# Performance work log

Measured on AMD Instinct MI355X. Metric: run time of the kernel, lower is better.

## Reference

```python
import jax, jax.numpy as jnp
import numpy as np

N = 50000      # nodes
E = 800000     # edges (before self-loops)
IN = 128       # in_channels
C = 64         # hidden_channels
HD = 4         # heads
SLOPE = 0.2    # GATConv leaky_relu negative slope
EPS_BN = 1e-5


def add_self_loops(edge_index, n):
    loop = jnp.arange(n, dtype=edge_index.dtype)
    return jnp.concatenate([edge_index, jnp.stack([loop, loop])], axis=1)


def gat_conv(x, edge_index, W, a_src, a_dst, bias, heads, out_c, concat, n):
    src, dst = edge_index[0], edge_index[1]
    h = (x @ W).reshape(n, heads, out_c)                 # [N,H,C]
    al_s = jnp.sum(h * a_src, axis=-1)                   # [N,H]
    al_d = jnp.sum(h * a_dst, axis=-1)                   # [N,H]
    e = jax.nn.leaky_relu(al_s[src] + al_d[dst], SLOPE)  # [Etot,H]
    m = jax.ops.segment_max(e, dst, num_segments=n)      # segment softmax (stable)
    ex = jnp.exp(e - m[dst])
    s = jax.ops.segment_sum(ex, dst, num_segments=n)
    alpha = ex / (s[dst] + 1e-16)                        # [Etot,H]
    out = jax.ops.segment_sum(h[src] * alpha[:, :, None], dst, num_segments=n)
    out = out.reshape(n, heads * out_c) if concat else out.mean(axis=1)
    return out + bias


def batch_norm(x, gamma, beta):
    mu = x.mean(axis=0)
    var = x.var(axis=0)
    return (x - mu) * jax.lax.rsqrt(var + EPS_BN) * gamma + beta


def setup_inputs() -> dict:
    key = jax.random.key(0)
    ks = jax.random.split(key, 24)
    f = lambda k, shp, sc: (jax.random.normal(k, shp, dtype=jnp.float32) * sc)
    HC = HD * C
    return {
        "x": f(ks[0], (N, IN), 1.0),
        "edge_index": jax.random.randint(ks[1], (2, E), 0, N, dtype=jnp.int64),
        # conv1: IN -> C, heads=HD, concat
        "W1": f(ks[2], (IN, HC), 0.05), "as1": f(ks[3], (HD, C), 0.05),
        "ad1": f(ks[4], (HD, C), 0.05), "b1": f(ks[5], (HC,), 0.02),
        "g1": jnp.ones((HC,), jnp.float32), "bb1": jnp.zeros((HC,), jnp.float32),
        # conv2: HC -> C, heads=HD, concat
        "W2": f(ks[6], (HC, HC), 0.05), "as2": f(ks[7], (HD, C), 0.05),
        "ad2": f(ks[8], (HD, C), 0.05), "b2": f(ks[9], (HC,), 0.02),
        "g2": jnp.ones((HC,), jnp.float32), "bb2": jnp.zeros((HC,), jnp.float32),
        # conv3: HC -> C, heads=1, mean
        "W3": f(ks[10], (HC, C), 0.05), "as3": f(ks[11], (1, C), 0.05),
        "ad3": f(ks[12], (1, C), 0.05), "b3": f(ks[13], (C,), 0.02),
        # skips
        "Ws1": f(ks[14], (IN, HC), 0.05), "bs1": f(ks[15], (HC,), 0.02),
        "Ws2": f(ks[16], (HC, C), 0.05), "bs2": f(ks[17], (C,), 0.02),
    }


def reference(x, edge_index, W1, as1, ad1, b1, g1, bb1,
              W2, as2, ad2, b2, g2, bb2,
              W3, as3, ad3, b3, Ws1, bs1, Ws2, bs2):
    ei = add_self_loops(edge_index, N)
    x_init = x @ Ws1 + bs1
    h = gat_conv(x, ei, W1, as1, ad1, b1, HD, C, True, N)
    h = jax.nn.elu(batch_norm(h, g1, bb1)) + x_init
    x_skip = h @ Ws2 + bs2
    h = gat_conv(h, ei, W2, as2, ad2, b2, HD, C, True, N)
    h = jax.nn.elu(batch_norm(h, g2, bb2))
    out = gat_conv(h, ei, W3, as3, ad3, b3, 1, C, False, N) + x_skip
    return out
```

## Files before the change

### kernel.cpp

```cpp
#include <hip/hip_runtime.h>
#include <hip/hip_bf16.h>
#include <cstdint>
#include <cstddef>


#define LRELU_SLOPE 0.2f

typedef __attribute__((ext_vector_type(8))) short short8;
typedef __attribute__((ext_vector_type(4))) float f32x4;

__device__ __forceinline__ float bf2f(unsigned short u) {
  union { unsigned int i; float f; } t; t.i = ((unsigned int)u) << 16; return t.f;
}
__device__ __forceinline__ unsigned short f2bf(float f) {
  __hip_bfloat16 h = __float2bfloat16(f);
  return *reinterpret_cast<unsigned short*>(&h);
}

template<int K, int WAVES_GAT, int WAVES_SKIP>
__global__ __launch_bounds__((WAVES_GAT + WAVES_SKIP) * 64)
void gemm_gat_fused(const unsigned short* __restrict__ A,
                    const unsigned short* __restrict__ BtH,
                    const unsigned short* __restrict__ BtS,
                    const float* __restrict__ a_s, const float* __restrict__ a_d,
                    const float* __restrict__ biasS,
                    unsigned short* __restrict__ Hout,
                    float* __restrict__ als, float* __restrict__ ald,
                    unsigned short* __restrict__ Sout, int M) {
  constexpr int NKS = K / 32;
  constexpr int NH  = WAVES_GAT * 64;
  constexpr int NS  = WAVES_SKIP * 64;
  const int wid  = threadIdx.x >> 6;
  const int lane = threadIdx.x & 63;
  const int r    = lane & 15;
  const int q    = lane >> 4;
  const int koff = q * 8;
  const bool isGat = wid < WAVES_GAT;
  const int colbase = isGat ? wid * 64 : (wid - WAVES_GAT) * 64;
  const unsigned short* Bt = isGat ? BtH : BtS;

  short8 b[4][NKS];
  #pragma unroll
  for (int nf = 0; nf < 4; ++nf)
    #pragma unroll
    for (int ks = 0; ks < NKS; ++ks)
      b[nf][ks] = *(const short8*)(Bt + (size_t)(colbase + nf * 16 + r) * K + ks * 32 + koff);

  float as4[4] = {}, ad4[4] = {};
  if (isGat) {
    #pragma unroll
    for (int nf = 0; nf < 4; ++nf) {
      as4[nf] = a_s[colbase + nf * 16 + r];
      ad4[nf] = a_d[colbase + nf * 16 + r];
    }
  }

  const int ntiles = (M + 15) >> 4;
  const int chunk = (ntiles + 7) >> 3;
  const int xcd   = blockIdx.x & 7;
  const int lo    = xcd * chunk;
  const int hi    = min(lo + chunk, ntiles);
  const int bstep = gridDim.x >> 3;
  for (int t = lo + (blockIdx.x >> 3); t < hi; t += bstep) {
    const int row = t * 16 + r;
    short8 a[NKS];
    #pragma unroll
    for (int ks = 0; ks < NKS; ++ks) {
      a[ks] = (short8)(short)0;
      if (row < M) a[ks] = *(const short8*)(A + (size_t)row * K + ks * 32 + koff);
    }
    f32x4 acc[4];
    #pragma unroll
    for (int nf = 0; nf < 4; ++nf) acc[nf] = (f32x4)0.0f;
    #pragma unroll
    for (int ks = 0; ks < NKS; ++ks)
      #pragma unroll
      for (int nf = 0; nf < 4; ++nf)
        acc[nf] = __builtin_amdgcn_mfma_f32_16x16x32_bf16(a[ks], b[nf][ks], acc[nf], 0, 0, 0);

    const int rbase = t * 16 + q * 4;
    if (isGat) {
      #pragma unroll
      for (int nf = 0; nf < 4; ++nf) {
        const int col = colbase + nf * 16 + r;
        #pragma unroll
        for (int i = 0; i < 4; ++i) {
          const int rr = rbase + i;
          if (rr < M) Hout[(size_t)rr * NH + col] = f2bf(acc[nf][i]);
        }
      }
      #pragma unroll
      for (int i = 0; i < 4; ++i) {
        float s = 0.f, d = 0.f;
        #pragma unroll
        for (int nf = 0; nf < 4; ++nf) {
          s = fmaf(acc[nf][i], as4[nf], s);
          d = fmaf(acc[nf][i], ad4[nf], d);
        }
        #pragma unroll
        for (int m = 8; m >= 1; m >>= 1) {
          s += __shfl_xor(s, m, 64);
          d += __shfl_xor(d, m, 64);
        }
        const int rr = rbase + i;
        if (r == 0 && rr < M) {
          als[(size_t)rr * WAVES_GAT + wid] = s;
          ald[(size_t)rr * WAVES_GAT + wid] = d;
        }
      }
    } else {
      #pragma unroll
      for (int nf = 0; nf < 4; ++nf) {
        const int col = colbase + nf * 16 + r;
        const float bs = biasS[col];
        #pragma unroll
        for (int i = 0; i < 4; ++i) {
          const int rr = rbase + i;
          if (rr < M) Sout[(size_t)rr * NS + col] = f2bf(acc[nf][i] + bs);
        }
      }
    }
  }
}

__global__ __launch_bounds__(256)
void gemm_gat3(const unsigned short* __restrict__ A, const unsigned short* __restrict__ Bt,
               const float* __restrict__ a_s, const float* __restrict__ a_d,
               unsigned short* __restrict__ Hout, float* __restrict__ als,
               float* __restrict__ ald, int M) {
  constexpr int K = 256, NKS = 8;
  const int wid  = threadIdx.x >> 6;
  const int lane = threadIdx.x & 63;
  const int r    = lane & 15;
  const int q    = lane >> 4;
  const int koff = q * 8;

  short8 b[4][NKS];
  #pragma unroll
  for (int nf = 0; nf < 4; ++nf)
    #pragma unroll
    for (int ks = 0; ks < NKS; ++ks)
      b[nf][ks] = *(const short8*)(Bt + (size_t)(nf * 16 + r) * K + ks * 32 + koff);
  float as4[4], ad4[4];
  #pragma unroll
  for (int nf = 0; nf < 4; ++nf) {
    as4[nf] = a_s[nf * 16 + r];
    ad4[nf] = a_d[nf * 16 + r];
  }

  const int ntiles = (M + 15) >> 4;
  const int chunk = (ntiles + 7) >> 3;
  const int xcd   = blockIdx.x & 7;
  const int lo    = xcd * chunk;
  const int hi    = min(lo + chunk, ntiles);
  const int bstep = (gridDim.x >> 3) * 4;
  for (int t = lo + (blockIdx.x >> 3) * 4 + wid; t < hi; t += bstep) {
    const int row = t * 16 + r;
    short8 a[NKS];
    #pragma unroll
    for (int ks = 0; ks < NKS; ++ks) {
      a[ks] = (short8)(short)0;
      if (row < M) a[ks] = *(const short8*)(A + (size_t)row * K + ks * 32 + koff);
    }
    f32x4 acc[4];
    #pragma unroll
    for (int nf = 0; nf < 4; ++nf) acc[nf] = (f32x4)0.0f;
    #pragma unroll
    for (int ks = 0; ks < NKS; ++ks)
      #pragma unroll
      for (int nf = 0; nf < 4; ++nf)
        acc[nf] = __builtin_amdgcn_mfma_f32_16x16x32_bf16(a[ks], b[nf][ks], acc[nf], 0, 0, 0);

    const int rbase = t * 16 + q * 4;
    #pragma unroll
    for (int nf = 0; nf < 4; ++nf) {
      const int col = nf * 16 + r;
      #pragma unroll
      for (int i = 0; i < 4; ++i) {
        const int rr = rbase + i;
        if (rr < M) Hout[(size_t)rr * 64 + col] = f2bf(acc[nf][i]);
      }
    }
    #pragma unroll
    for (int i = 0; i < 4; ++i) {
      float s = 0.f, d = 0.f;
      #pragma unroll
      for (int nf = 0; nf < 4; ++nf) {
        s = fmaf(acc[nf][i], as4[nf], s);
        d = fmaf(acc[nf][i], ad4[nf], d);
      }
      #pragma unroll
      for (int m = 8; m >= 1; m >>= 1) {
        s += __shfl_xor(s, m, 64);
        d += __shfl_xor(d, m, 64);
      }
      const int rr = rbase + i;
      if (r == 0 && rr < M) { als[rr] = s; ald[rr] = d; }
    }
  }
}

__global__ __launch_bounds__(256)
void prep_all(const float* __restrict__ x,
              const float* __restrict__ W1, const float* __restrict__ Ws1,
              const float* __restrict__ W2, const float* __restrict__ Ws2,
              const float* __restrict__ W3,
              unsigned short* __restrict__ xb,
              unsigned short* __restrict__ W1t, unsigned short* __restrict__ Ws1t,
              unsigned short* __restrict__ W2t, unsigned short* __restrict__ Ws2t,
              unsigned short* __restrict__ W3t, int n) {
  int idx = blockIdx.x * blockDim.x + threadIdx.x;
  const int nx = n * 32;
  if (idx < nx) {
    float4 v = ((const float4*)x)[idx];
    ushort4 o;
    o.x = f2bf(v.x); o.y = f2bf(v.y); o.z = f2bf(v.z); o.w = f2bf(v.w);
    ((ushort4*)xb)[idx] = o;
    return;
  }
  idx -= nx;
  if (idx < 256 * 128) { int nn = idx >> 7, kk = idx & 127; W1t[idx]  = f2bf(W1[kk * 256 + nn]);  return; }
  idx -= 256 * 128;
  if (idx < 256 * 128) { int nn = idx >> 7, kk = idx & 127; Ws1t[idx] = f2bf(Ws1[kk * 256 + nn]); return; }
  idx -= 256 * 128;
  if (idx < 256 * 256) { int nn = idx >> 8, kk = idx & 255; W2t[idx]  = f2bf(W2[kk * 256 + nn]);  return; }
  idx -= 256 * 256;
  if (idx < 64 * 256)  { int nn = idx >> 8, kk = idx & 255; Ws2t[idx] = f2bf(Ws2[kk * 64 + nn]);  return; }
  idx -= 64 * 256;
  if (idx < 64 * 256)  { int nn = idx >> 8, kk = idx & 255; W3t[idx]  = f2bf(W3[kk * 64 + nn]); }
}

__global__ void count_edges(const int* __restrict__ ei, int E, int* __restrict__ counts) {
  int i = blockIdx.x * blockDim.x + threadIdx.x;
  if (i < E) atomicAdd(&counts[ei[E + i]], 1);
}
__global__ void scan_block(const int* __restrict__ in, int* __restrict__ out,
                           int* __restrict__ bsums, int n) {
  __shared__ int tmp[256];
  int t = threadIdx.x;
  int gid = blockIdx.x * 256 + t;
  int v = (gid < n) ? in[gid] : 0;
  tmp[t] = v;
  __syncthreads();
  #pragma unroll
  for (int off = 1; off < 256; off <<= 1) {
    int x = (t >= off) ? tmp[t - off] : 0;
    __syncthreads();
    tmp[t] += x;
    __syncthreads();
  }
  if (gid < n) out[gid] = tmp[t] - v;
  if (t == 255) bsums[blockIdx.x] = tmp[255];
}
__global__ void scan_tops(const int* __restrict__ bsums, int* __restrict__ boffs, int nb) {
  __shared__ int tmp[256];
  int t = threadIdx.x;
  int v = (t < nb) ? bsums[t] : 0;
  tmp[t] = v;
  __syncthreads();
  #pragma unroll
  for (int off = 1; off < 256; off <<= 1) {
    int x = (t >= off) ? tmp[t - off] : 0;
    __syncthreads();
    tmp[t] += x;
    __syncthreads();
  }
  if (t < nb) boffs[t] = tmp[t] - v;
}
__global__ void scan_add(int* __restrict__ rp, const int* __restrict__ boffs,
                         int n, int etot) {
  int gid = blockIdx.x * 256 + threadIdx.x;
  if (gid < n) rp[gid] += boffs[blockIdx.x];
  if (gid == 0) rp[n] = etot;
}
__global__ void fill_edges(const int* __restrict__ ei, int E, const int* __restrict__ rp,
                           int* __restrict__ cursor, int* __restrict__ csr) {
  int i = blockIdx.x * blockDim.x + threadIdx.x;
  if (i < E) {
    int d = ei[E + i];
    int s = ei[i];
    int pos = rp[d] + atomicAdd(&cursor[d], 1);
    csr[pos] = s;
  }
}

template<int HEADS, int HCt, bool OUT_BF16>
__global__ __launch_bounds__(256)
void gat_aggregate(const unsigned short* __restrict__ H, const float* __restrict__ als,
                   const float* __restrict__ ald, const int* __restrict__ rp,
                   const int* __restrict__ csr, const float* __restrict__ bias,
                   const unsigned short* __restrict__ skip, void* __restrict__ out, int n) {
  constexpr int CPL = HCt / 64;
  int w = (blockIdx.x * blockDim.x + threadIdx.x) >> 6;
  int lane = threadIdx.x & 63;
  if (w >= n) return;
  const int beg = rp[w], end = rp[w + 1];
  const int myhead = (HEADS == 1) ? 0 : (lane >> 4);
  const float adh = ald[(size_t)w * HEADS + myhead];

  auto att = [&](int s) -> float {
    float e = als[(size_t)s * HEADS + myhead] + adh;
    e = fmaxf(e, LRELU_SLOPE * e);
    return __expf(e);
  };

  float acc[CPL];
  float ssum = att(w);
  {
    const unsigned short* hp = H + (size_t)w * HCt + lane * CPL;
    if constexpr (CPL == 4) {
      ushort4 hv = *(const ushort4*)hp;
      acc[0] = ssum * bf2f(hv.x); acc[1] = ssum * bf2f(hv.y);
      acc[2] = ssum * bf2f(hv.z); acc[3] = ssum * bf2f(hv.w);
    } else {
      acc[0] = ssum * bf2f(hp[0]);
    }
  }

  int j = beg;
  for (; j + 8 <= end; j += 8) {
    int sidx[8];
    #pragma unroll
    for (int u = 0; u < 8; ++u) sidx[u] = csr[j + u];
    if constexpr (CPL == 4) {
      ushort4 hv[8];
      #pragma unroll
      for (int u = 0; u < 8; ++u)
        hv[u] = *(const ushort4*)(H + (size_t)sidx[u] * HCt + lane * 4);
      float ex[8];
      #pragma unroll
      for (int u = 0; u < 8; ++u) ex[u] = att(sidx[u]);
      #pragma unroll
      for (int u = 0; u < 8; ++u) {
        ssum += ex[u];
        acc[0] = fmaf(ex[u], bf2f(hv[u].x), acc[0]);
        acc[1] = fmaf(ex[u], bf2f(hv[u].y), acc[1]);
        acc[2] = fmaf(ex[u], bf2f(hv[u].z), acc[2]);
        acc[3] = fmaf(ex[u], bf2f(hv[u].w), acc[3]);
      }
    } else {
      unsigned short hv[8];
      #pragma unroll
      for (int u = 0; u < 8; ++u) hv[u] = H[(size_t)sidx[u] * HCt + lane];
      float ex[8];
      #pragma unroll
      for (int u = 0; u < 8; ++u) ex[u] = att(sidx[u]);
      #pragma unroll
      for (int u = 0; u < 8; ++u) {
        ssum += ex[u];
        acc[0] = fmaf(ex[u], bf2f(hv[u]), acc[0]);
      }
    }
  }
  for (; j + 4 <= end; j += 4) {
    int sidx[4];
    #pragma unroll
    for (int u = 0; u < 4; ++u) sidx[u] = csr[j + u];
    float ex[4];
    #pragma unroll
    for (int u = 0; u < 4; ++u) ex[u] = att(sidx[u]);
    if constexpr (CPL == 4) {
      ushort4 hv[4];
      #pragma unroll
      for (int u = 0; u < 4; ++u)
        hv[u] = *(const ushort4*)(H + (size_t)sidx[u] * HCt + lane * 4);
      #pragma unroll
      for (int u = 0; u < 4; ++u) {
        ssum += ex[u];
        acc[0] = fmaf(ex[u], bf2f(hv[u].x), acc[0]);
        acc[1] = fmaf(ex[u], bf2f(hv[u].y), acc[1]);
        acc[2] = fmaf(ex[u], bf2f(hv[u].z), acc[2]);
        acc[3] = fmaf(ex[u], bf2f(hv[u].w), acc[3]);
      }
    } else {
      unsigned short hv[4];
      #pragma unroll
      for (int u = 0; u < 4; ++u) hv[u] = H[(size_t)sidx[u] * HCt + lane];
      #pragma unroll
      for (int u = 0; u < 4; ++u) {
        ssum += ex[u];
        acc[0] = fmaf(ex[u], bf2f(hv[u]), acc[0]);
      }
    }
  }
  for (; j < end; ++j) {
    const int s = csr[j];
    const float ex = att(s);
    ssum += ex;
    const unsigned short* hp = H + (size_t)s * HCt + lane * CPL;
    if constexpr (CPL == 4) {
      ushort4 hv = *(const ushort4*)hp;
      acc[0] = fmaf(ex, bf2f(hv.x), acc[0]);
      acc[1] = fmaf(ex, bf2f(hv.y), acc[1]);
      acc[2] = fmaf(ex, bf2f(hv.z), acc[2]);
      acc[3] = fmaf(ex, bf2f(hv.w), acc[3]);
    } else {
      acc[0] = fmaf(ex, bf2f(hp[0]), acc[0]);
    }
  }

  const float inv = 1.f / (ssum + 1e-16f);
  #pragma unroll
  for (int c = 0; c < CPL; ++c) {
    int ch = lane * CPL + c;
    float v = acc[c] * inv + bias[ch];
    if (skip) v += bf2f(skip[(size_t)w * HCt + ch]);
    if constexpr (OUT_BF16)
      ((unsigned short*)out)[(size_t)w * HCt + ch] = f2bf(v);
    else
      ((float*)out)[(size_t)w * HCt + ch] = v;
  }
}

__global__ __launch_bounds__(256)
void bn_stats(const unsigned short* __restrict__ X, float* __restrict__ sums, int n) {
  int c = threadIdx.x;
  float s = 0.f, q = 0.f;
  for (int r = blockIdx.x; r < n; r += gridDim.x) {
    float v = bf2f(X[(size_t)r * 256 + c]);
    s += v;
    q = fmaf(v, v, q);
  }
  atomicAdd(&sums[c], s);
  atomicAdd(&sums[256 + c], q);
}
__global__ void bn_finalize(const float* __restrict__ sums, const float* __restrict__ gamma,
                            const float* __restrict__ beta, float* __restrict__ scsh,
                            int n) {
  int c = threadIdx.x;
  if (c < 256) {
    float mean = sums[c] / (float)n;
    float var = sums[256 + c] / (float)n - mean * mean;
    float sc = gamma[c] * rsqrtf(var + 1e-5f);
    scsh[c] = sc;
    scsh[256 + c] = beta[c] - mean * sc;
  }
}
__global__ __launch_bounds__(256)
void bn_apply_elu(const unsigned short* __restrict__ X, const float* __restrict__ scsh,
                  const unsigned short* __restrict__ skip, unsigned short* __restrict__ Y,
                  int total) {
  int i4 = blockIdx.x * blockDim.x + threadIdx.x;
  if (i4 * 4 >= total) return;
  ushort4 xv = ((const ushort4*)X)[i4];
  int cb = (i4 * 4) & 255;
  float4 sc = *(const float4*)(scsh + cb);
  float4 sh = *(const float4*)(scsh + 256 + cb);
  float4 y;
  y.x = fmaf(bf2f(xv.x), sc.x, sh.x);
  y.y = fmaf(bf2f(xv.y), sc.y, sh.y);
  y.z = fmaf(bf2f(xv.z), sc.z, sh.z);
  y.w = fmaf(bf2f(xv.w), sc.w, sh.w);
  y.x = (y.x > 0.f) ? y.x : expm1f(y.x);
  y.y = (y.y > 0.f) ? y.y : expm1f(y.y);
  y.z = (y.z > 0.f) ? y.z : expm1f(y.z);
  y.w = (y.w > 0.f) ? y.w : expm1f(y.w);
  if (skip) {
    ushort4 s4 = ((const ushort4*)skip)[i4];
    y.x += bf2f(s4.x); y.y += bf2f(s4.y); y.z += bf2f(s4.z); y.w += bf2f(s4.w);
  }
  ushort4 o;
  o.x = f2bf(y.x); o.y = f2bf(y.y); o.z = f2bf(y.z); o.w = f2bf(y.w);
  ((ushort4*)Y)[i4] = o;
}

extern "C" void kernel_launch(void* const* d_in, const int* in_sizes, int n_in,
                              void* d_out, int out_size, void* d_ws, size_t ws_size,
                              hipStream_t stream) {
  const float* x   = (const float*)d_in[0];
  const int*   ei  = (const int*)d_in[1];
  const float* W1  = (const float*)d_in[2];
  const float* as1 = (const float*)d_in[3];
  const float* ad1 = (const float*)d_in[4];
  const float* b1  = (const float*)d_in[5];
  const float* g1  = (const float*)d_in[6];
  const float* bb1 = (const float*)d_in[7];
  const float* W2  = (const float*)d_in[8];
  const float* as2 = (const float*)d_in[9];
  const float* ad2 = (const float*)d_in[10];
  const float* b2  = (const float*)d_in[11];
  const float* g2  = (const float*)d_in[12];
  const float* bb2 = (const float*)d_in[13];
  const float* W3  = (const float*)d_in[14];
  const float* as3 = (const float*)d_in[15];
  const float* ad3 = (const float*)d_in[16];
  const float* b3  = (const float*)d_in[17];
  const float* Ws1 = (const float*)d_in[18];
  const float* bs1 = (const float*)d_in[19];
  const float* Ws2 = (const float*)d_in[20];
  const float* bs2 = (const float*)d_in[21];

  const int n = in_sizes[0] / 128;
  const int E = in_sizes[1] / 2;

  char* wsp = (char*)d_ws;
  auto carve = [&](size_t bytes) -> void* {
    void* p = (void*)wsp;
    wsp += (bytes + 255) & ~(size_t)255;
    return p;
  };
  unsigned short* Hb  = (unsigned short*)carve((size_t)n * 256 * 2);
  unsigned short* hb  = (unsigned short*)carve((size_t)n * 256 * 2);
  unsigned short* xbD = (unsigned short*)carve((size_t)n * 128 * 2);
  unsigned short* xb  = xbD;
  unsigned short* D   = xbD;
  unsigned short* Bv  = (unsigned short*)carve((size_t)n * 256 * 2);
  unsigned short* Cv  = (unsigned short*)carve((size_t)n * 256 * 2);
  float* als  = (float*)carve((size_t)n * 4 * 4);
  float* ald  = (float*)carve((size_t)n * 4 * 4);
  int*   rp   = (int*)carve((size_t)(n + 1) * 4);
  int*   cnt  = (int*)carve((size_t)n * 4);
  int*   bsums= (int*)carve(256 * 4);
  int*   boffs= (int*)carve(256 * 4);
  int*   csr  = (int*)carve((size_t)E * 4);
  float* bnb  = (float*)carve(4 * 256 * 4);
  float* sums = bnb;
  float* scsh = bnb + 512;
  unsigned short* W1t  = (unsigned short*)carve(128 * 256 * 2);
  unsigned short* Ws1t = (unsigned short*)carve(128 * 256 * 2);
  unsigned short* W2t  = (unsigned short*)carve(256 * 256 * 2);
  unsigned short* Ws2t = (unsigned short*)carve(256 * 64 * 2);
  unsigned short* W3t  = (unsigned short*)carve(256 * 64 * 2);

  const int NB = (n + 255) / 256;
  const int EB = (E + 255) / 256;

  hipMemsetAsync(cnt, 0, (size_t)n * 4, stream);
  count_edges<<<EB, 256, 0, stream>>>(ei, E, cnt);
  scan_block<<<NB, 256, 0, stream>>>(cnt, rp, bsums, n);
  scan_tops<<<1, 256, 0, stream>>>(bsums, boffs, NB);
  scan_add<<<NB, 256, 0, stream>>>(rp, boffs, n, E);
  hipMemsetAsync(cnt, 0, (size_t)n * 4, stream);
  fill_edges<<<EB, 256, 0, stream>>>(ei, E, rp, cnt, csr);

  {
    const int total = n * 32 + 2 * 256 * 128 + 256 * 256 + 2 * 64 * 256;
    prep_all<<<(total + 255) / 256, 256, 0, stream>>>(x, W1, Ws1, W2, Ws2, W3,
                                                      xb, W1t, Ws1t, W2t, Ws2t, W3t, n);
  }

  const int wgrid = (n * 64 + 255) / 256;
  const int egrid = (n * 256 / 4 + 255) / 256;

  gemm_gat_fused<128, 4, 4><<<512, 512, 0, stream>>>(
      xb, W1t, Ws1t, as1, ad1, bs1, Hb, als, ald, Bv, n);
  gat_aggregate<4, 256, true><<<wgrid, 256, 0, stream>>>(Hb, als, ald, rp, csr, b1,
                                                         nullptr, Cv, n);
  hipMemsetAsync(sums, 0, 512 * 4, stream);
  bn_stats<<<256, 256, 0, stream>>>(Cv, sums, n);
  bn_finalize<<<1, 256, 0, stream>>>(sums, g1, bb1, scsh, n);
  bn_apply_elu<<<egrid, 256, 0, stream>>>(Cv, scsh, Bv, hb, n * 256);

  gemm_gat_fused<256, 4, 1><<<512, 320, 0, stream>>>(
      hb, W2t, Ws2t, as2, ad2, bs2, Hb, als, ald, D, n);
  gat_aggregate<4, 256, true><<<wgrid, 256, 0, stream>>>(Hb, als, ald, rp, csr, b2,
                                                         nullptr, Cv, n);
  hipMemsetAsync(sums, 0, 512 * 4, stream);
  bn_stats<<<256, 256, 0, stream>>>(Cv, sums, n);
  bn_finalize<<<1, 256, 0, stream>>>(sums, g2, bb2, scsh, n);
  bn_apply_elu<<<egrid, 256, 0, stream>>>(Cv, scsh, nullptr, hb, n * 256);

  gemm_gat3<<<512, 256, 0, stream>>>(hb, W3t, as3, ad3, Hb, als, ald, n);
  gat_aggregate<1, 64, false><<<wgrid, 256, 0, stream>>>(Hb, als, ald, rp, csr, b3, D,
                                                         d_out, n);
}
```

Baseline: 515.2 us.

## Precompute per-edge attention exponentials in separate kernel before aggregation

```diff
diff --git a/kernel.cpp b/kernel.cpp
--- a/kernel.cpp
+++ b/kernel.cpp
@@ -274,39 +274,60 @@
   if (gid == 0) rp[n] = etot;
 }
 __global__ void fill_edges(const int* __restrict__ ei, int E, const int* __restrict__ rp,
-                           int* __restrict__ cursor, int* __restrict__ csr) {
+                           int* __restrict__ cursor, int* __restrict__ csr,
+                           int* __restrict__ dstv) {
   int i = blockIdx.x * blockDim.x + threadIdx.x;
   if (i < E) {
     int d = ei[E + i];
     int s = ei[i];
     int pos = rp[d] + atomicAdd(&cursor[d], 1);
     csr[pos] = s;
+    dstv[pos] = d;
+  }
+}
+
+template<int HEADS>
+__global__ __launch_bounds__(256)
+void edge_att(const int* __restrict__ csr, const int* __restrict__ dstv,
+              const float* __restrict__ als, const float* __restrict__ ald,
+              unsigned short* __restrict__ exf, int E) {
+  int t = blockIdx.x * blockDim.x + threadIdx.x;
+  if constexpr (HEADS == 4) {
+    int j = t >> 2, h = t & 3;
+    if (j >= E) return;
+    int s = csr[j], d = dstv[j];
+    float e = als[(size_t)s * 4 + h] + ald[(size_t)d * 4 + h];
+    e = fmaxf(e, LRELU_SLOPE * e);
+    exf[t] = f2bf(__expf(e));
+  } else {
+    if (t >= E) return;
+    int s = csr[t], d = dstv[t];
+    float e = als[s] + ald[d];
+    e = fmaxf(e, LRELU_SLOPE * e);
+    exf[t] = f2bf(__expf(e));
   }
 }
 
 template<int HEADS, int HCt, bool OUT_BF16>
 __global__ __launch_bounds__(256)
-void gat_aggregate(const unsigned short* __restrict__ H, const float* __restrict__ als,
-                   const float* __restrict__ ald, const int* __restrict__ rp,
-                   const int* __restrict__ csr, const float* __restrict__ bias,
-                   const unsigned short* __restrict__ skip, void* __restrict__ out, int n) {
+void gat_aggregate(const unsigned short* __restrict__ H, const unsigned short* __restrict__ exf,
+                   const float* __restrict__ als, const float* __restrict__ ald,
+                   const int* __restrict__ rp, const int* __restrict__ csr,
+                   const float* __restrict__ bias, const unsigned short* __restrict__ skip,
+                   void* __restrict__ out, int n) {
   constexpr int CPL = HCt / 64;
   int w = (blockIdx.x * blockDim.x + threadIdx.x) >> 6;
   int lane = threadIdx.x & 63;
   if (w >= n) return;
   const int beg = rp[w], end = rp[w + 1];
   const int myhead = (HEADS == 1) ? 0 : (lane >> 4);
-  const float adh = ald[(size_t)w * HEADS + myhead];
-
-  auto att = [&](int s) -> float {
-    float e = als[(size_t)s * HEADS + myhead] + adh;
+
+  float acc[CPL];
+  float ssum;
+  {
+    float e = als[(size_t)w * HEADS + myhead] + ald[(size_t)w * HEADS + myhead];
     e = fmaxf(e, LRELU_SLOPE * e);
-    return __expf(e);
-  };
-
-  float acc[CPL];
-  float ssum = att(w);
-  {
+    ssum = __expf(e);
     const unsigned short* hp = H + (size_t)w * HCt + lane * CPL;
     if constexpr (CPL == 4) {
       ushort4 hv = *(const ushort4*)hp;
@@ -322,14 +343,14 @@
     int sidx[8];
     #pragma unroll
     for (int u = 0; u < 8; ++u) sidx[u] = csr[j + u];
+    float ex[8];
+    #pragma unroll
+    for (int u = 0; u < 8; ++u) ex[u] = bf2f(exf[(size_t)(j + u) * HEADS + myhead]);
     if constexpr (CPL == 4) {
       ushort4 hv[8];
       #pragma unroll
       for (int u = 0; u < 8; ++u)
         hv[u] = *(const ushort4*)(H + (size_t)sidx[u] * HCt + lane * 4);
-      float ex[8];
-      #pragma unroll
-      for (int u = 0; u < 8; ++u) ex[u] = att(sidx[u]);
       #pragma unroll
       for (int u = 0; u < 8; ++u) {
         ssum += ex[u];
@@ -342,9 +363,6 @@
       unsigned short hv[8];
       #pragma unroll
       for (int u = 0; u < 8; ++u) hv[u] = H[(size_t)sidx[u] * HCt + lane];
-      float ex[8];
-      #pragma unroll
-      for (int u = 0; u < 8; ++u) ex[u] = att(sidx[u]);
       #pragma unroll
       for (int u = 0; u < 8; ++u) {
         ssum += ex[u];
@@ -358,7 +376,7 @@
     for (int u = 0; u < 4; ++u) sidx[u] = csr[j + u];
     float ex[4];
     #pragma unroll
-    for (int u = 0; u < 4; ++u) ex[u] = att(sidx[u]);
+    for (int u = 0; u < 4; ++u) ex[u] = bf2f(exf[(size_t)(j + u) * HEADS + myhead]);
     if constexpr (CPL == 4) {
       ushort4 hv[4];
       #pragma unroll
@@ -385,7 +403,7 @@
   }
   for (; j < end; ++j) {
     const int s = csr[j];
-    const float ex = att(s);
+    const float ex = bf2f(exf[(size_t)j * HEADS + myhead]);
     ssum += ex;
     const unsigned short* hp = H + (size_t)s * HCt + lane * CPL;
     if constexpr (CPL == 4) {
@@ -513,6 +531,8 @@
   int*   bsums= (int*)carve(256 * 4);
   int*   boffs= (int*)carve(256 * 4);
   int*   csr  = (int*)carve((size_t)E * 4);
+  int*   dstv = (int*)carve((size_t)E * 4);
+  unsigned short* exf = (unsigned short*)carve((size_t)E * 4 * 2);
   float* bnb  = (float*)carve(4 * 256 * 4);
   float* sums = bnb;
   float* scsh = bnb + 512;
@@ -531,7 +551,7 @@
   scan_tops<<<1, 256, 0, stream>>>(bsums, boffs, NB);
   scan_add<<<NB, 256, 0, stream>>>(rp, boffs, n, E);
   hipMemsetAsync(cnt, 0, (size_t)n * 4, stream);
-  fill_edges<<<EB, 256, 0, stream>>>(ei, E, rp, cnt, csr);
+  fill_edges<<<EB, 256, 0, stream>>>(ei, E, rp, cnt, csr, dstv);
 
   {
     const int total = n * 32 + 2 * 256 * 128 + 256 * 256 + 2 * 64 * 256;
@@ -541,11 +561,14 @@
 
   const int wgrid = (n * 64 + 255) / 256;
   const int egrid = (n * 256 / 4 + 255) / 256;
+  const int e4grid = (E * 4 + 255) / 256;
+  const int e1grid = (E + 255) / 256;
 
   gemm_gat_fused<128, 4, 4><<<512, 512, 0, stream>>>(
       xb, W1t, Ws1t, as1, ad1, bs1, Hb, als, ald, Bv, n);
-  gat_aggregate<4, 256, true><<<wgrid, 256, 0, stream>>>(Hb, als, ald, rp, csr, b1,
-                                                         nullptr, Cv, n);
+  edge_att<4><<<e4grid, 256, 0, stream>>>(csr, dstv, als, ald, exf, E);
+  gat_aggregate<4, 256, true><<<wgrid, 256, 0, stream>>>(Hb, exf, als, ald, rp, csr,
+                                                         b1, nullptr, Cv, n);
   hipMemsetAsync(sums, 0, 512 * 4, stream);
   bn_stats<<<256, 256, 0, stream>>>(Cv, sums, n);
   bn_finalize<<<1, 256, 0, stream>>>(sums, g1, bb1, scsh, n);
@@ -553,14 +576,16 @@
 
   gemm_gat_fused<256, 4, 1><<<512, 320, 0, stream>>>(
       hb, W2t, Ws2t, as2, ad2, bs2, Hb, als, ald, D, n);
-  gat_aggregate<4, 256, true><<<wgrid, 256, 0, stream>>>(Hb, als, ald, rp, csr, b2,
-                                                         nullptr, Cv, n);
+  edge_att<4><<<e4grid, 256, 0, stream>>>(csr, dstv, als, ald, exf, E);
+  gat_aggregate<4, 256, true><<<wgrid, 256, 0, stream>>>(Hb, exf, als, ald, rp, csr,
+                                                         b2, nullptr, Cv, n);
   hipMemsetAsync(sums, 0, 512 * 4, stream);
   bn_stats<<<256, 256, 0, stream>>>(Cv, sums, n);
   bn_finalize<<<1, 256, 0, stream>>>(sums, g2, bb2, scsh, n);
   bn_apply_elu<<<egrid, 256, 0, stream>>>(Cv, scsh, nullptr, hb, n * 256);
 
   gemm_gat3<<<512, 256, 0, stream>>>(hb, W3t, as3, ad3, Hb, als, ald, n);
-  gat_aggregate<1, 64, false><<<wgrid, 256, 0, stream>>>(Hb, als, ald, rp, csr, b3, D,
-                                                         d_out, n);
-}
+  edge_att<1><<<e1grid, 256, 0, stream>>>(csr, dstv, als, ald, exf, E);
+  gat_aggregate<1, 64, false><<<wgrid, 256, 0, stream>>>(Hb, exf, als, ald, rp, csr,
+                                                         b3, D, d_out, n);
+}
```

After: 540.2 us. +4.9%, slower.

## Partition edge counting and CSR fill by destination range across block groups

Applied to the files above, without the earlier changes.

```diff
diff --git a/kernel.cpp b/kernel.cpp
--- a/kernel.cpp
+++ b/kernel.cpp
@@ -230,9 +230,16 @@
   if (idx < 64 * 256)  { int nn = idx >> 8, kk = idx & 255; W3t[idx]  = f2bf(W3[kk * 64 + nn]); }
 }
 
-__global__ void count_edges(const int* __restrict__ ei, int E, int* __restrict__ counts) {
-  int i = blockIdx.x * blockDim.x + threadIdx.x;
-  if (i < E) atomicAdd(&counts[ei[E + i]], 1);
+__global__ void count_edges(const int* __restrict__ ei, int E, int* __restrict__ counts,
+                            int n) {
+  const int g = blockIdx.x & 7;
+  const int chunk = (n + 7) >> 3;
+  const int lo = g * chunk, hi = min(lo + chunk, n);
+  const int stride = (gridDim.x >> 3) * blockDim.x;
+  for (int i = (blockIdx.x >> 3) * blockDim.x + threadIdx.x; i < E; i += stride) {
+    int d = ei[E + i];
+    if (d >= lo && d < hi) atomicAdd(&counts[d], 1);
+  }
 }
 __global__ void scan_block(const int* __restrict__ in, int* __restrict__ out,
                            int* __restrict__ bsums, int n) {
@@ -274,13 +281,17 @@
   if (gid == 0) rp[n] = etot;
 }
 __global__ void fill_edges(const int* __restrict__ ei, int E, const int* __restrict__ rp,
-                           int* __restrict__ cursor, int* __restrict__ csr) {
-  int i = blockIdx.x * blockDim.x + threadIdx.x;
-  if (i < E) {
+                           int* __restrict__ cursor, int* __restrict__ csr, int n) {
+  const int g = blockIdx.x & 7;
+  const int chunk = (n + 7) >> 3;
+  const int lo = g * chunk, hi = min(lo + chunk, n);
+  const int stride = (gridDim.x >> 3) * blockDim.x;
+  for (int i = (blockIdx.x >> 3) * blockDim.x + threadIdx.x; i < E; i += stride) {
     int d = ei[E + i];
-    int s = ei[i];
-    int pos = rp[d] + atomicAdd(&cursor[d], 1);
-    csr[pos] = s;
+    if (d >= lo && d < hi) {
+      int pos = rp[d] + atomicAdd(&cursor[d], 1);
+      csr[pos] = ei[i];
+    }
   }
 }
 
@@ -523,15 +534,14 @@
   unsigned short* W3t  = (unsigned short*)carve(256 * 64 * 2);
 
   const int NB = (n + 255) / 256;
-  const int EB = (E + 255) / 256;
 
   hipMemsetAsync(cnt, 0, (size_t)n * 4, stream);
-  count_edges<<<EB, 256, 0, stream>>>(ei, E, cnt);
+  count_edges<<<2048, 256, 0, stream>>>(ei, E, cnt, n);
   scan_block<<<NB, 256, 0, stream>>>(cnt, rp, bsums, n);
   scan_tops<<<1, 256, 0, stream>>>(bsums, boffs, NB);
   scan_add<<<NB, 256, 0, stream>>>(rp, boffs, n, E);
   hipMemsetAsync(cnt, 0, (size_t)n * 4, stream);
-  fill_edges<<<EB, 256, 0, stream>>>(ei, E, rp, cnt, csr);
+  fill_edges<<<2048, 256, 0, stream>>>(ei, E, rp, cnt, csr, n);
 
   {
     const int total = n * 32 + 2 * 256 * 128 + 256 * 256 + 2 * 64 * 256;
```

Result: no change. 513.2 us (-0.4%).
